# Kernel optimization log

Measured on AMD Instinct MI355X. Metric: run time of the kernel, lower is better.

The kernel has to match this reference:

```python
import jax, jax.numpy as jnp
import numpy as np
import math

NUM_HIDDEN = 512

def setup_inputs() -> dict:
    key = jax.random.key(0)
    k1, k2 = jax.random.split(key)
    a = jax.random.normal(k1, (8, 2048, NUM_HIDDEN), dtype=jnp.float32)
    b = jax.random.normal(k2, (8, 2048, NUM_HIDDEN), dtype=jnp.float32)
    return {"a": a, "b": b}

def reference(a, b):
    # simi_matrix: [B, La, Lb] = a @ b^T / sqrt(H)
    scale = 1.0 / math.sqrt(NUM_HIDDEN)
    simi = jnp.einsum('bld,bmd->blm', a, b) * scale
    norm_weight = jax.nn.softmax(simi, axis=2)
    # up_1: [B, La, H] = attn @ b + residual a
    up_1 = jnp.einsum('blm,bmd->bld', norm_weight, b) + a
    return up_1
```

## Files before the change

kernel.cpp:

```cpp
#include <hip/hip_runtime.h>
#include <hip/hip_bf16.h>

#define D 512
#define NSEQ 2048
#define NB 8
#define QBLK 64
#define KVBLK 64
#define NTHREADS 512
#define NT (NSEQ / KVBLK)
#define ROWE 2112
#define BUFE (16 * ROWE)
#define PROWP 72
#define CROWP 68
#define DEFER_THR 8.0f

typedef __attribute__((ext_vector_type(8))) short bf16x8;
typedef __attribute__((ext_vector_type(4))) float f32x4;
typedef __attribute__((ext_vector_type(4))) unsigned short u16x4;
typedef __attribute__((ext_vector_type(4))) int i32x4;

static __device__ __forceinline__ unsigned short f2b(float f) {
  unsigned u = __builtin_bit_cast(unsigned, f);
  return (unsigned short)((u + 0x7FFFu + ((u >> 16) & 1u)) >> 16);
}

__global__ __launch_bounds__(256) void conv_dual(const float* __restrict__ in,
                                                 unsigned short* __restrict__ b16,
                                                 unsigned short* __restrict__ bT) {
  __shared__ unsigned short tile[64 * CROWP];
  const int bid = blockIdx.x;
  const int batch = bid >> 8;
  const int rem = bid & 255;
  const int kvt = rem >> 3;
  const int dt  = rem & 7;
  const int t = threadIdx.x;
  const int r = t >> 2;
  const int c = (t & 3) * 16;

  const float* src = in + ((size_t)batch * NSEQ + kvt * 64 + r) * D + dt * 64 + c;
  unsigned short* o16 = b16 + ((size_t)batch * NSEQ + kvt * 64 + r) * D + dt * 64 + c;

  float4 v0 = *reinterpret_cast<const float4*>(src);
  float4 v1 = *reinterpret_cast<const float4*>(src + 4);
  float4 v2 = *reinterpret_cast<const float4*>(src + 8);
  float4 v3 = *reinterpret_cast<const float4*>(src + 12);
  bf16x8 h0, h1;
  h0[0] = (short)f2b(v0.x); h0[1] = (short)f2b(v0.y);
  h0[2] = (short)f2b(v0.z); h0[3] = (short)f2b(v0.w);
  h0[4] = (short)f2b(v1.x); h0[5] = (short)f2b(v1.y);
  h0[6] = (short)f2b(v1.z); h0[7] = (short)f2b(v1.w);
  h1[0] = (short)f2b(v2.x); h1[1] = (short)f2b(v2.y);
  h1[2] = (short)f2b(v2.z); h1[3] = (short)f2b(v2.w);
  h1[4] = (short)f2b(v3.x); h1[5] = (short)f2b(v3.y);
  h1[6] = (short)f2b(v3.z); h1[7] = (short)f2b(v3.w);
  *reinterpret_cast<bf16x8*>(o16)     = h0;
  *reinterpret_cast<bf16x8*>(o16 + 8) = h1;
  #pragma unroll
  for (int i = 0; i < 4; ++i) {
    u16x4 w;
    w[0] = (unsigned short)((i < 2 ? h0 : h1)[(i & 1) * 4 + 0]);
    w[1] = (unsigned short)((i < 2 ? h0 : h1)[(i & 1) * 4 + 1]);
    w[2] = (unsigned short)((i < 2 ? h0 : h1)[(i & 1) * 4 + 2]);
    w[3] = (unsigned short)((i < 2 ? h0 : h1)[(i & 1) * 4 + 3]);
    *reinterpret_cast<u16x4*>(&tile[r * CROWP + c + i * 4]) = w;
  }
  __syncthreads();

  const int w  = t >> 6;
  const int dr = t & 63;
  unsigned short* oT = bT + (size_t)batch * D * NSEQ
                          + (size_t)(dt * 64 + dr) * NSEQ + kvt * 64 + w * 16;
  unsigned short g[16];
  #pragma unroll
  for (int i = 0; i < 16; ++i)
    g[i] = tile[(w * 16 + i) * CROWP + dr];
  bf16x8 p0, p1;
  #pragma unroll
  for (int i = 0; i < 8; ++i) { p0[i] = (short)g[i]; p1[i] = (short)g[8 + i]; }
  *reinterpret_cast<bf16x8*>(oT)     = p0;
  *reinterpret_cast<bf16x8*>(oT + 8) = p1;
}

__global__ __launch_bounds__(NTHREADS, 1)
void attn_v18(const float* __restrict__ A, const unsigned short* __restrict__ B16,
              const unsigned short* __restrict__ T16, float* __restrict__ Out) {
  __shared__ __align__(16) unsigned short Bs[BUFE];
  __shared__ __align__(16) unsigned short Bt[D * KVBLK];
  __shared__ __align__(16) unsigned short Ps[QBLK * PROWP];
  __shared__ float mS[QBLK];
  __shared__ float lS[QBLK];
  __shared__ float aS[QBLK];
  __shared__ float pmaxS[128];
  __shared__ float psumS[128];
  __shared__ __align__(16) int flagS[8];

  const int tid  = threadIdx.x;
  const int wid  = tid >> 6;
  const int lane = tid & 63;
  const int l16  = lane & 15;
  const int g4   = lane >> 4;

  const int batch = blockIdx.x & 7;
  const int qt    = blockIdx.x >> 3;
  const int qbase = qt * QBLK;

  const float*          Ab = A   + (size_t)batch * NSEQ * D;
  const unsigned short* Kb = B16 + (size_t)batch * NSEQ * D;
  const unsigned short* Tb = T16 + (size_t)batch * D * NSEQ;
  float*                Ob = Out + (size_t)batch * NSEQ * D;

  const float scale = 0.04419417382415922f;

  const int qi = wid >> 1;
  const int kp = wid & 1;

  const float* Arow = Ab + (size_t)(qbase + qi * 16 + l16) * D;
  bf16x8 qf[16];
  #pragma unroll
  for (int ks = 0; ks < 16; ++ks) {
    int d0 = ks * 32 + g4 * 8;
    float4 v0 = *reinterpret_cast<const float4*>(Arow + d0);
    float4 v1 = *reinterpret_cast<const float4*>(Arow + d0 + 4);
    bf16x8 f;
    f[0] = (short)f2b(v0.x * scale); f[1] = (short)f2b(v0.y * scale);
    f[2] = (short)f2b(v0.z * scale); f[3] = (short)f2b(v0.w * scale);
    f[4] = (short)f2b(v1.x * scale); f[5] = (short)f2b(v1.y * scale);
    f[6] = (short)f2b(v1.z * scale); f[7] = (short)f2b(v1.w * scale);
    qf[ks] = f;
  }
  if (tid < QBLK) { mS[tid] = -1e30f; lS[tid] = 0.f; }

  f32x4 acc[4][4];
  #pragma unroll
  for (int mi = 0; mi < 4; ++mi)
    #pragma unroll
    for (int ni = 0; ni < 4; ++ni)
      acc[mi][ni] = (f32x4){0.f, 0.f, 0.f, 0.f};

  #pragma unroll
  for (int c = 0; c < 8; ++c) {
    int id = wid * 8 + c;
    int g = id >> 2, q = id & 3;
    const unsigned short* src = Kb
        + (size_t)(g * 4 + ((lane >> 1) & 3)) * D
        + q * 128 + (lane >> 3) * 16 + (lane & 1) * 8;
    unsigned short* dst = &Bs[g * ROWE + q * 512];
    __builtin_amdgcn_global_load_lds(
        (const __attribute__((address_space(1))) void*)src,
        (__attribute__((address_space(3))) void*)dst, 16, 0, 0);
  }
  #pragma unroll
  for (int c = 0; c < 8; ++c) {
    int drow = wid * 64 + c * 8 + (lane >> 3);
    int chunk = (lane & 7) ^ ((lane >> 3) & 7);
    const unsigned short* src = Tb + (size_t)drow * NSEQ + chunk * 8;
    unsigned short* dst = (unsigned short*)&Bt[(wid * 64 + c * 8) * KVBLK];
    __builtin_amdgcn_global_load_lds(
        (const __attribute__((address_space(1))) void*)src,
        (__attribute__((address_space(3))) void*)dst, 16, 0, 0);
  }
  asm volatile("s_waitcnt vmcnt(0)" ::: "memory");
  asm volatile("s_waitcnt lgkmcnt(0)" ::: "memory");
  __builtin_amdgcn_s_barrier();

  const int bbase0 = ((kp * 2) * 4 + (l16 >> 2)) * ROWE + (l16 & 3) * 16 + (g4 & 1) * 8;
  const int bbase1 = bbase0 + 4 * ROWE;

  for (int kt = 0; kt < NT; ++kt) {
    f32x4 s0 = {0.f, 0.f, 0.f, 0.f};
    f32x4 s1 = {0.f, 0.f, 0.f, 0.f};
    __builtin_amdgcn_s_setprio(1);
    #pragma unroll
    for (int ks = 0; ks < 16; ++ks) {
      const int ro = (ks * 2 + (g4 >> 1)) * 64;
      const bf16x8 b0 = *reinterpret_cast<const bf16x8*>(&Bs[bbase0 + ro]);
      const bf16x8 b1 = *reinterpret_cast<const bf16x8*>(&Bs[bbase1 + ro]);
      s0 = __builtin_amdgcn_mfma_f32_16x16x32_bf16(b0, qf[ks], s0, 0, 0, 0);
      s1 = __builtin_amdgcn_mfma_f32_16x16x32_bf16(b1, qf[ks], s1, 0, 0, 0);
    }
    __builtin_amdgcn_s_setprio(0);

    {
      float m01 = fmaxf(s0[0], s0[1]), m23 = fmaxf(s0[2], s0[3]);
      float m45 = fmaxf(s1[0], s1[1]), m67 = fmaxf(s1[2], s1[3]);
      float mloc = fmaxf(fmaxf(m01, m23), fmaxf(m45, m67));
      mloc = fmaxf(mloc, __shfl_xor(mloc, 16));
      mloc = fmaxf(mloc, __shfl_xor(mloc, 32));
      if (lane < 16) pmaxS[qi * 32 + kp * 16 + lane] = mloc;
      asm volatile("s_waitcnt lgkmcnt(0)" ::: "memory");
      __builtin_amdgcn_s_barrier();

      if (kt + 1 < NT) {
        const unsigned short* Kt = Kb + (size_t)(kt + 1) * KVBLK * D;
        #pragma unroll
        for (int c = 0; c < 8; ++c) {
          int id = wid * 8 + c;
          int g = id >> 2, q = id & 3;
          const unsigned short* src = Kt
              + (size_t)(g * 4 + ((lane >> 1) & 3)) * D
              + q * 128 + (lane >> 3) * 16 + (lane & 1) * 8;
          unsigned short* dst = &Bs[g * ROWE + q * 512];
          __builtin_amdgcn_global_load_lds(
              (const __attribute__((address_space(1))) void*)src,
              (__attribute__((address_space(3))) void*)dst, 16, 0, 0);
        }
      }

      float mpart = pmaxS[qi * 32 + (kp ^ 1) * 16 + l16];
      float mcomb = fmaxf(mloc, mpart);
      float mold = mS[qi * 16 + l16];
      int defer = (mcomb <= mold + DEFER_THR) ? 1 : 0;
      float mnew = defer ? mold : mcomb;
      float al = defer ? 1.0f : __expf(mold - mnew);

      float rowsum = 0.f;
      u16x4 w0, w1;
      #pragma unroll
      for (int r = 0; r < 4; ++r) {
        float p = __expf(s0[r] - mnew);
        rowsum += p;
        w0[r] = f2b(p);
      }
      #pragma unroll
      for (int r = 0; r < 4; ++r) {
        float p = __expf(s1[r] - mnew);
        rowsum += p;
        w1[r] = f2b(p);
      }
      const int prow = (qi * 16 + l16) * PROWP + 32 * kp + 4 * g4;
      *reinterpret_cast<u16x4*>(&Ps[prow])      = w0;
      *reinterpret_cast<u16x4*>(&Ps[prow + 16]) = w1;

      rowsum += __shfl_xor(rowsum, 16);
      rowsum += __shfl_xor(rowsum, 32);
      if (lane < 16) psumS[qi * 32 + kp * 16 + lane] = rowsum;
      int wave_defer = __all(defer);
      if (kp == 0 && lane < 16) {
        mS[qi * 16 + lane] = mnew;
        aS[qi * 16 + lane] = al;
      }
      if (lane == 0) flagS[wid] = wave_defer;

      asm volatile("s_waitcnt lgkmcnt(0)" ::: "memory");
      if (kt + 1 < NT) {
        asm volatile("s_waitcnt vmcnt(8)" ::: "memory");
      } else {
        asm volatile("s_waitcnt vmcnt(0)" ::: "memory");
      }
      __builtin_amdgcn_s_barrier();

      if (kp == 0 && lane < 16) {
        float pp = psumS[qi * 32 + 16 + lane];
        lS[qi * 16 + lane] = lS[qi * 16 + lane] * al + rowsum + pp;
      }
    }

    {
      i32x4 f0 = *reinterpret_cast<const i32x4*>(&flagS[0]);
      i32x4 f1 = *reinterpret_cast<const i32x4*>(&flagS[4]);
      int allskip = f0[0] & f0[1] & f0[2] & f0[3] & f1[0] & f1[1] & f1[2] & f1[3];
      if (!allskip) {
        #pragma unroll
        for (int mi = 0; mi < 4; ++mi) {
          float a = aS[mi * 16 + l16];
          #pragma unroll
          for (int ni = 0; ni < 4; ++ni)
            #pragma unroll
            for (int r = 0; r < 4; ++r)
              acc[mi][ni][r] *= a;
        }
      }

      const char* Bc = (const char*)&Bt[0];
      __builtin_amdgcn_s_setprio(1);
      #pragma unroll
      for (int ks = 0; ks < 2; ++ks) {
        bf16x8 pf[4];
        #pragma unroll
        for (int mi = 0; mi < 4; ++mi)
          pf[mi] = *reinterpret_cast<const bf16x8*>(
              &Ps[(mi * 16 + l16) * PROWP + ks * 32 + g4 * 8]);
        #pragma unroll
        for (int ni = 0; ni < 4; ++ni) {
          int row = wid * 64 + ni * 16 + l16;
          int swz = (ks * 4 + g4) ^ (l16 & 7);
          const bf16x8 vf = *reinterpret_cast<const bf16x8*>(Bc + row * 128 + swz * 16);
          #pragma unroll
          for (int mi = 0; mi < 4; ++mi)
            acc[mi][ni] = __builtin_amdgcn_mfma_f32_16x16x32_bf16(vf, pf[mi], acc[mi][ni], 0, 0, 0);
        }
      }
      __builtin_amdgcn_s_setprio(0);
    }
    asm volatile("s_waitcnt lgkmcnt(0)" ::: "memory");

    if (kt + 1 < NT) {
      #pragma unroll
      for (int c = 0; c < 8; ++c) {
        int drow = wid * 64 + c * 8 + (lane >> 3);
        int chunk = (lane & 7) ^ ((lane >> 3) & 7);
        const unsigned short* src = Tb + (size_t)drow * NSEQ + (kt + 1) * KVBLK + chunk * 8;
        unsigned short* dst = (unsigned short*)&Bt[(wid * 64 + c * 8) * KVBLK];
        __builtin_amdgcn_global_load_lds(
            (const __attribute__((address_space(1))) void*)src,
            (__attribute__((address_space(3))) void*)dst, 16, 0, 0);
      }
      asm volatile("s_waitcnt vmcnt(8)" ::: "memory");
    }
    __builtin_amdgcn_s_barrier();
  }

  #pragma unroll
  for (int mi = 0; mi < 4; ++mi) {
    float rl = 1.0f / lS[mi * 16 + l16];
    int q = qbase + mi * 16 + l16;
    #pragma unroll
    for (int ni = 0; ni < 4; ++ni) {
      int d = wid * 64 + ni * 16 + g4 * 4;
      const float4 av = *reinterpret_cast<const float4*>(Ab + (size_t)q * D + d);
      float4 o;
      o.x = acc[mi][ni][0] * rl + av.x;
      o.y = acc[mi][ni][1] * rl + av.y;
      o.z = acc[mi][ni][2] * rl + av.z;
      o.w = acc[mi][ni][3] * rl + av.w;
      *reinterpret_cast<float4*>(Ob + (size_t)q * D + d) = o;
    }
  }
}

#define FQBLK 32
#define FSROWP (64 + 4)
#define FPROWP (64 + 8)
__global__ __launch_bounds__(NTHREADS, 2)
void attn_fb(const float* __restrict__ A, const float* __restrict__ B32,
             float* __restrict__ Out) {
  __shared__ __align__(16) unsigned short Bs[BUFE];
  __shared__ float Ss[FQBLK * FSROWP];
  __shared__ unsigned short Ps[FQBLK * FPROWP];
  __shared__ float mS[FQBLK];
  __shared__ float lS[FQBLK];
  __shared__ float aS[FQBLK];

  const int tid  = threadIdx.x;
  const int wid  = tid >> 6;
  const int lane = tid & 63;
  const int l16  = lane & 15;
  const int g4   = lane >> 4;

  const int batch = blockIdx.x & 7;
  const int qt    = blockIdx.x >> 3;
  const int qbase = qt * FQBLK;

  const float* Ab   = A   + (size_t)batch * NSEQ * D;
  const float* Bb32 = B32 + (size_t)batch * NSEQ * D;
  float*       Ob   = Out + (size_t)batch * NSEQ * D;

  const float scale = 0.04419417382415922f;

  const int qi = wid >> 2;
  const int ki = wid & 3;

  const float* Arow = Ab + (size_t)(qbase + qi * 16 + l16) * D;
  bf16x8 qf[16];
  #pragma unroll
  for (int ks = 0; ks < 16; ++ks) {
    int d0 = ks * 32 + g4 * 8;
    float4 v0 = *reinterpret_cast<const float4*>(Arow + d0);
    float4 v1 = *reinterpret_cast<const float4*>(Arow + d0 + 4);
    bf16x8 f;
    f[0] = (short)f2b(v0.x * scale); f[1] = (short)f2b(v0.y * scale);
    f[2] = (short)f2b(v0.z * scale); f[3] = (short)f2b(v0.w * scale);
    f[4] = (short)f2b(v1.x * scale); f[5] = (short)f2b(v1.y * scale);
    f[6] = (short)f2b(v1.z * scale); f[7] = (short)f2b(v1.w * scale);
    qf[ks] = f;
  }
  if (tid < FQBLK) { mS[tid] = -1e30f; lS[tid] = 0.f; }

  f32x4 acc[2][4];
  #pragma unroll
  for (int mi = 0; mi < 2; ++mi)
    #pragma unroll
    for (int ni = 0; ni < 4; ++ni)
      acc[mi][ni] = (f32x4){0.f, 0.f, 0.f, 0.f};

  for (int kt = 0; kt < NT; ++kt) {
    __builtin_amdgcn_s_barrier();
    const float* Bt2 = Bb32 + (size_t)kt * KVBLK * D;
    #pragma unroll
    for (int c = 0; c < 8; ++c) {
      int id = wid * 8 + c;
      int g = id >> 2, q = id & 3;
      int kv = g * 4 + ((lane >> 1) & 3);
      int d  = q * 128 + (lane >> 3) * 16 + (lane & 1) * 8;
      const float* s = Bt2 + (size_t)kv * D + d;
      float4 v0 = *reinterpret_cast<const float4*>(s);
      float4 v1 = *reinterpret_cast<const float4*>(s + 4);
      bf16x8 h;
      h[0] = (short)f2b(v0.x); h[1] = (short)f2b(v0.y);
      h[2] = (short)f2b(v0.z); h[3] = (short)f2b(v0.w);
      h[4] = (short)f2b(v1.x); h[5] = (short)f2b(v1.y);
      h[6] = (short)f2b(v1.z); h[7] = (short)f2b(v1.w);
      *reinterpret_cast<bf16x8*>(&Bs[g * ROWE + q * 512 + lane * 8]) = h;
    }
    asm volatile("s_waitcnt lgkmcnt(0)" ::: "memory");
    __builtin_amdgcn_s_barrier();

    {
      f32x4 s = {0.f, 0.f, 0.f, 0.f};
      const int bbase = (ki * 4 + (l16 >> 2)) * ROWE + (l16 & 3) * 16 + (g4 & 1) * 8;
      #pragma unroll
      for (int ks = 0; ks < 16; ++ks) {
        const bf16x8 bf = *reinterpret_cast<const bf16x8*>(
            &Bs[bbase + (ks * 2 + (g4 >> 1)) * 64]);
        s = __builtin_amdgcn_mfma_f32_16x16x32_bf16(qf[ks], bf, s, 0, 0, 0);
      }
      #pragma unroll
      for (int r = 0; r < 4; ++r)
        Ss[(qi * 16 + g4 * 4 + r) * FSROWP + ki * 16 + l16] = s[r];
    }
    asm volatile("s_waitcnt lgkmcnt(0)" ::: "memory");
    __builtin_amdgcn_s_barrier();

    {
      int row = wid * 4 + g4;
      float sv[4];
      float mloc = -1e30f;
      #pragma unroll
      for (int j = 0; j < 4; ++j) {
        sv[j] = Ss[row * FSROWP + l16 + 16 * j];
        mloc = fmaxf(mloc, sv[j]);
      }
      #pragma unroll
      for (int off = 1; off < 16; off <<= 1)
        mloc = fmaxf(mloc, __shfl_xor(mloc, off));
      float mold = mS[row];
      float mnew = fmaxf(mold, mloc);
      float al = __expf(mold - mnew);
      float psum = 0.f;
      #pragma unroll
      for (int j = 0; j < 4; ++j) {
        float p = __expf(sv[j] - mnew);
        psum += p;
        Ps[row * FPROWP + l16 + 16 * j] = f2b(p);
      }
      #pragma unroll
      for (int off = 1; off < 16; off <<= 1)
        psum += __shfl_xor(psum, off);
      if (l16 == 0) {
        mS[row] = mnew;
        lS[row] = lS[row] * al + psum;
        aS[row] = al;
      }
    }
    asm volatile("s_waitcnt lgkmcnt(0)" ::: "memory");
    __builtin_amdgcn_s_barrier();

    {
      #pragma unroll
      for (int mi = 0; mi < 2; ++mi)
        #pragma unroll
        for (int r = 0; r < 4; ++r) {
          float a = aS[mi * 16 + g4 * 4 + r];
          #pragma unroll
          for (int ni = 0; ni < 4; ++ni)
            acc[mi][ni][r] *= a;
        }

      #pragma unroll
      for (int ks = 0; ks < 2; ++ks) {
        bf16x8 pf[2];
        #pragma unroll
        for (int mi = 0; mi < 2; ++mi)
          pf[mi] = *reinterpret_cast<const bf16x8*>(
              &Ps[(mi * 16 + l16) * FPROWP + ks * 32 + g4 * 8]);
        #pragma unroll
        for (int ni = 0; ni < 4; ++ni) {
          bf16x8 vv;
          #pragma unroll
          for (int j = 0; j < 8; ++j)
            vv[j] = (short)Bs[(ks * 8 + g4 * 2 + (j >> 2)) * ROWE
                              + (wid * 4 + ni) * 64 + (j & 3) * 16 + l16];
          #pragma unroll
          for (int mi = 0; mi < 2; ++mi)
            acc[mi][ni] = __builtin_amdgcn_mfma_f32_16x16x32_bf16(pf[mi], vv, acc[mi][ni], 0, 0, 0);
        }
      }
    }
  }

  #pragma unroll
  for (int mi = 0; mi < 2; ++mi)
    #pragma unroll
    for (int r = 0; r < 4; ++r) {
      float rl = 1.0f / lS[mi * 16 + g4 * 4 + r];
      #pragma unroll
      for (int ni = 0; ni < 4; ++ni) {
        int q = qbase + mi * 16 + g4 * 4 + r;
        int d = wid * 64 + ni * 16 + l16;
        size_t off = (size_t)q * D + d;
        Ob[off] = acc[mi][ni][r] * rl + Ab[off];
      }
    }
}

extern "C" void kernel_launch(void* const* d_in, const int* in_sizes, int n_in,
                              void* d_out, int out_size, void* d_ws, size_t ws_size,
                              hipStream_t stream) {
  const float* a = (const float*)d_in[0];
  const float* b = (const float*)d_in[1];
  float* out = (float*)d_out;
  const size_t one = (size_t)NB * NSEQ * D * sizeof(unsigned short);
  dim3 block(NTHREADS);
  if (ws_size >= 2 * one) {
    unsigned short* b16 = (unsigned short*)d_ws;
    unsigned short* bT  = b16 + (size_t)NB * NSEQ * D;
    conv_dual<<<NB * 256, 256, 0, stream>>>(b, b16, bT);
    dim3 grid(NB * (NSEQ / QBLK));
    attn_v18<<<grid, block, 0, stream>>>(a, b16, bT, out);
  } else {
    dim3 grid(NB * (NSEQ / FQBLK));
    attn_fb<<<grid, block, 0, stream>>>(a, b, out);
  }
}
```

Measured before the change: 131.1 us.

## Remap QK^T wave tiling so each wave shares one K fragment across two query tiles

Each wave now owns one 16-row KV slice and two 16-row query tiles, instead of one query tile and two KV slices. Each LDS read of K feeds two MFMAs, halving K fragment reads from LDS in the score loop. The cost is twice the Q fragments held in registers (32 bf16x8), which raises VGPR pressure. The row max and sum reduction becomes a four-way merge across KV slices through shared memory.

After: 218.0 us. 1.66x slower.

```diff
diff --git a/kernel.cpp b/kernel.cpp
--- a/kernel.cpp
+++ b/kernel.cpp
@@ -82,7 +82,7 @@
 }
 
 __global__ __launch_bounds__(NTHREADS, 1)
-void attn_v18(const float* __restrict__ A, const unsigned short* __restrict__ B16,
+void attn_v19(const float* __restrict__ A, const unsigned short* __restrict__ B16,
               const unsigned short* __restrict__ T16, float* __restrict__ Out) {
   __shared__ __align__(16) unsigned short Bs[BUFE];
   __shared__ __align__(16) unsigned short Bt[D * KVBLK];
@@ -90,8 +90,8 @@
   __shared__ float mS[QBLK];
   __shared__ float lS[QBLK];
   __shared__ float aS[QBLK];
-  __shared__ float pmaxS[128];
-  __shared__ float psumS[128];
+  __shared__ float pmaxS[4 * 64];
+  __shared__ float psumS[4 * 64];
   __shared__ __align__(16) int flagS[8];
 
   const int tid  = threadIdx.x;
@@ -111,22 +111,33 @@
 
   const float scale = 0.04419417382415922f;
 
-  const int qi = wid >> 1;
-  const int kp = wid & 1;
-
-  const float* Arow = Ab + (size_t)(qbase + qi * 16 + l16) * D;
-  bf16x8 qf[16];
-  #pragma unroll
-  for (int ks = 0; ks < 16; ++ks) {
-    int d0 = ks * 32 + g4 * 8;
-    float4 v0 = *reinterpret_cast<const float4*>(Arow + d0);
-    float4 v1 = *reinterpret_cast<const float4*>(Arow + d0 + 4);
-    bf16x8 f;
-    f[0] = (short)f2b(v0.x * scale); f[1] = (short)f2b(v0.y * scale);
-    f[2] = (short)f2b(v0.z * scale); f[3] = (short)f2b(v0.w * scale);
-    f[4] = (short)f2b(v1.x * scale); f[5] = (short)f2b(v1.y * scale);
-    f[6] = (short)f2b(v1.z * scale); f[7] = (short)f2b(v1.w * scale);
-    qf[ks] = f;
+  const int kvt = wid >> 1;
+  const int qp  = wid & 1;
+  const int t0  = qp * 2, t1 = qp * 2 + 1;
+
+  bf16x8 qf0[16], qf1[16];
+  {
+    const float* Ar0 = Ab + (size_t)(qbase + t0 * 16 + l16) * D;
+    const float* Ar1 = Ab + (size_t)(qbase + t1 * 16 + l16) * D;
+    #pragma unroll
+    for (int ks = 0; ks < 16; ++ks) {
+      int d0 = ks * 32 + g4 * 8;
+      float4 a0 = *reinterpret_cast<const float4*>(Ar0 + d0);
+      float4 a1 = *reinterpret_cast<const float4*>(Ar0 + d0 + 4);
+      float4 b0 = *reinterpret_cast<const float4*>(Ar1 + d0);
+      float4 b1 = *reinterpret_cast<const float4*>(Ar1 + d0 + 4);
+      bf16x8 f0, f1;
+      f0[0] = (short)f2b(a0.x * scale); f0[1] = (short)f2b(a0.y * scale);
+      f0[2] = (short)f2b(a0.z * scale); f0[3] = (short)f2b(a0.w * scale);
+      f0[4] = (short)f2b(a1.x * scale); f0[5] = (short)f2b(a1.y * scale);
+      f0[6] = (short)f2b(a1.z * scale); f0[7] = (short)f2b(a1.w * scale);
+      f1[0] = (short)f2b(b0.x * scale); f1[1] = (short)f2b(b0.y * scale);
+      f1[2] = (short)f2b(b0.z * scale); f1[3] = (short)f2b(b0.w * scale);
+      f1[4] = (short)f2b(b1.x * scale); f1[5] = (short)f2b(b1.y * scale);
+      f1[6] = (short)f2b(b1.z * scale); f1[7] = (short)f2b(b1.w * scale);
+      qf0[ks] = f0;
+      qf1[ks] = f1;
+    }
   }
   if (tid < QBLK) { mS[tid] = -1e30f; lS[tid] = 0.f; }
 
@@ -163,8 +174,7 @@
   asm volatile("s_waitcnt lgkmcnt(0)" ::: "memory");
   __builtin_amdgcn_s_barrier();
 
-  const int bbase0 = ((kp * 2) * 4 + (l16 >> 2)) * ROWE + (l16 & 3) * 16 + (g4 & 1) * 8;
-  const int bbase1 = bbase0 + 4 * ROWE;
+  const int bbase = (kvt * 4 + (l16 >> 2)) * ROWE + (l16 & 3) * 16 + (g4 & 1) * 8;
 
   for (int kt = 0; kt < NT; ++kt) {
     f32x4 s0 = {0.f, 0.f, 0.f, 0.f};
@@ -173,86 +183,114 @@
     #pragma unroll
     for (int ks = 0; ks < 16; ++ks) {
       const int ro = (ks * 2 + (g4 >> 1)) * 64;
-      const bf16x8 b0 = *reinterpret_cast<const bf16x8*>(&Bs[bbase0 + ro]);
-      const bf16x8 b1 = *reinterpret_cast<const bf16x8*>(&Bs[bbase1 + ro]);
-      s0 = __builtin_amdgcn_mfma_f32_16x16x32_bf16(b0, qf[ks], s0, 0, 0, 0);
-      s1 = __builtin_amdgcn_mfma_f32_16x16x32_bf16(b1, qf[ks], s1, 0, 0, 0);
+      const bf16x8 b = *reinterpret_cast<const bf16x8*>(&Bs[bbase + ro]);
+      s0 = __builtin_amdgcn_mfma_f32_16x16x32_bf16(b, qf0[ks], s0, 0, 0, 0);
+      s1 = __builtin_amdgcn_mfma_f32_16x16x32_bf16(b, qf1[ks], s1, 0, 0, 0);
     }
     __builtin_amdgcn_s_setprio(0);
 
+    float mloc0, mloc1;
     {
-      float m01 = fmaxf(s0[0], s0[1]), m23 = fmaxf(s0[2], s0[3]);
-      float m45 = fmaxf(s1[0], s1[1]), m67 = fmaxf(s1[2], s1[3]);
-      float mloc = fmaxf(fmaxf(m01, m23), fmaxf(m45, m67));
-      mloc = fmaxf(mloc, __shfl_xor(mloc, 16));
-      mloc = fmaxf(mloc, __shfl_xor(mloc, 32));
-      if (lane < 16) pmaxS[qi * 32 + kp * 16 + lane] = mloc;
-      asm volatile("s_waitcnt lgkmcnt(0)" ::: "memory");
-      __builtin_amdgcn_s_barrier();
-
-      if (kt + 1 < NT) {
-        const unsigned short* Kt = Kb + (size_t)(kt + 1) * KVBLK * D;
-        #pragma unroll
-        for (int c = 0; c < 8; ++c) {
-          int id = wid * 8 + c;
-          int g = id >> 2, q = id & 3;
-          const unsigned short* src = Kt
-              + (size_t)(g * 4 + ((lane >> 1) & 3)) * D
-              + q * 128 + (lane >> 3) * 16 + (lane & 1) * 8;
-          unsigned short* dst = &Bs[g * ROWE + q * 512];
-          __builtin_amdgcn_global_load_lds(
-              (const __attribute__((address_space(1))) void*)src,
-              (__attribute__((address_space(3))) void*)dst, 16, 0, 0);
-        }
-      }
-
-      float mpart = pmaxS[qi * 32 + (kp ^ 1) * 16 + l16];
-      float mcomb = fmaxf(mloc, mpart);
-      float mold = mS[qi * 16 + l16];
-      int defer = (mcomb <= mold + DEFER_THR) ? 1 : 0;
-      float mnew = defer ? mold : mcomb;
-      float al = defer ? 1.0f : __expf(mold - mnew);
-
-      float rowsum = 0.f;
+      float a01 = fmaxf(s0[0], s0[1]), a23 = fmaxf(s0[2], s0[3]);
+      float b01 = fmaxf(s1[0], s1[1]), b23 = fmaxf(s1[2], s1[3]);
+      mloc0 = fmaxf(a01, a23);
+      mloc1 = fmaxf(b01, b23);
+      mloc0 = fmaxf(mloc0, __shfl_xor(mloc0, 16));
+      mloc0 = fmaxf(mloc0, __shfl_xor(mloc0, 32));
+      mloc1 = fmaxf(mloc1, __shfl_xor(mloc1, 16));
+      mloc1 = fmaxf(mloc1, __shfl_xor(mloc1, 32));
+      if (lane < 32) {
+        int t = (lane < 16) ? t0 : t1;
+        float v = (lane < 16) ? mloc0 : mloc1;
+        pmaxS[kvt * 64 + t * 16 + l16] = v;
+      }
+    }
+    asm volatile("s_waitcnt lgkmcnt(0)" ::: "memory");
+    __builtin_amdgcn_s_barrier();
+
+    if (kt + 1 < NT) {
+      const unsigned short* Kt = Kb + (size_t)(kt + 1) * KVBLK * D;
+      #pragma unroll
+      for (int c = 0; c < 8; ++c) {
+        int id = wid * 8 + c;
+        int g = id >> 2, q = id & 3;
+        const unsigned short* src = Kt
+            + (size_t)(g * 4 + ((lane >> 1) & 3)) * D
+            + q * 128 + (lane >> 3) * 16 + (lane & 1) * 8;
+        unsigned short* dst = &Bs[g * ROWE + q * 512];
+        __builtin_amdgcn_global_load_lds(
+            (const __attribute__((address_space(1))) void*)src,
+            (__attribute__((address_space(3))) void*)dst, 16, 0, 0);
+      }
+    }
+
+    float al0, al1, rowsum0, rowsum1;
+    int defer0, defer1;
+    {
+      const int row0 = t0 * 16 + l16, row1 = t1 * 16 + l16;
+      float p0a = pmaxS[0 * 64 + row0], p0b = pmaxS[1 * 64 + row0];
+      float p0c = pmaxS[2 * 64 + row0], p0d = pmaxS[3 * 64 + row0];
+      float p1a = pmaxS[0 * 64 + row1], p1b = pmaxS[1 * 64 + row1];
+      float p1c = pmaxS[2 * 64 + row1], p1d = pmaxS[3 * 64 + row1];
+      float mc0 = fmaxf(fmaxf(p0a, p0b), fmaxf(p0c, p0d));
+      float mc1 = fmaxf(fmaxf(p1a, p1b), fmaxf(p1c, p1d));
+      float mold0 = mS[row0], mold1 = mS[row1];
+      defer0 = (mc0 <= mold0 + DEFER_THR) ? 1 : 0;
+      defer1 = (mc1 <= mold1 + DEFER_THR) ? 1 : 0;
+      float mnew0 = defer0 ? mold0 : mc0;
+      float mnew1 = defer1 ? mold1 : mc1;
+      al0 = defer0 ? 1.0f : __expf(mold0 - mnew0);
+      al1 = defer1 ? 1.0f : __expf(mold1 - mnew1);
+
+      rowsum0 = 0.f; rowsum1 = 0.f;
       u16x4 w0, w1;
       #pragma unroll
       for (int r = 0; r < 4; ++r) {
-        float p = __expf(s0[r] - mnew);
-        rowsum += p;
+        float p = __expf(s0[r] - mnew0);
+        rowsum0 += p;
         w0[r] = f2b(p);
       }
       #pragma unroll
       for (int r = 0; r < 4; ++r) {
-        float p = __expf(s1[r] - mnew);
-        rowsum += p;
+        float p = __expf(s1[r] - mnew1);
+        rowsum1 += p;
         w1[r] = f2b(p);
       }
-      const int prow = (qi * 16 + l16) * PROWP + 32 * kp + 4 * g4;
-      *reinterpret_cast<u16x4*>(&Ps[prow])      = w0;
-      *reinterpret_cast<u16x4*>(&Ps[prow + 16]) = w1;
-
-      rowsum += __shfl_xor(rowsum, 16);
-      rowsum += __shfl_xor(rowsum, 32);
-      if (lane < 16) psumS[qi * 32 + kp * 16 + lane] = rowsum;
-      int wave_defer = __all(defer);
-      if (kp == 0 && lane < 16) {
-        mS[qi * 16 + lane] = mnew;
-        aS[qi * 16 + lane] = al;
+      const int kvoff = kvt * 16 + 4 * g4;
+      *reinterpret_cast<u16x4*>(&Ps[row0 * PROWP + kvoff]) = w0;
+      *reinterpret_cast<u16x4*>(&Ps[row1 * PROWP + kvoff]) = w1;
+
+      rowsum0 += __shfl_xor(rowsum0, 16);
+      rowsum0 += __shfl_xor(rowsum0, 32);
+      rowsum1 += __shfl_xor(rowsum1, 16);
+      rowsum1 += __shfl_xor(rowsum1, 32);
+      if (lane < 32) {
+        int t = (lane < 16) ? t0 : t1;
+        float v = (lane < 16) ? rowsum0 : rowsum1;
+        psumS[kvt * 64 + t * 16 + l16] = v;
+      }
+      int wave_defer = __all(defer0 & defer1);
+      if (kvt == 0 && lane < 32) {
+        int row = ((lane < 16) ? t0 : t1) * 16 + l16;
+        mS[row] = (lane < 16) ? mnew0 : mnew1;
+        aS[row] = (lane < 16) ? al0 : al1;
       }
       if (lane == 0) flagS[wid] = wave_defer;
-
-      asm volatile("s_waitcnt lgkmcnt(0)" ::: "memory");
-      if (kt + 1 < NT) {
-        asm volatile("s_waitcnt vmcnt(8)" ::: "memory");
-      } else {
-        asm volatile("s_waitcnt vmcnt(0)" ::: "memory");
-      }
-      __builtin_amdgcn_s_barrier();
-
-      if (kp == 0 && lane < 16) {
-        float pp = psumS[qi * 32 + 16 + lane];
-        lS[qi * 16 + lane] = lS[qi * 16 + lane] * al + rowsum + pp;
-      }
+    }
+    asm volatile("s_waitcnt lgkmcnt(0)" ::: "memory");
+    if (kt + 1 < NT) {
+      asm volatile("s_waitcnt vmcnt(8)" ::: "memory");
+    } else {
+      asm volatile("s_waitcnt vmcnt(0)" ::: "memory");
+    }
+    __builtin_amdgcn_s_barrier();
+
+    if (kvt == 0 && lane < 32) {
+      int row = ((lane < 16) ? t0 : t1) * 16 + l16;
+      float al = (lane < 16) ? al0 : al1;
+      float sum4 = psumS[0 * 64 + row] + psumS[1 * 64 + row]
+                 + psumS[2 * 64 + row] + psumS[3 * 64 + row];
+      lS[row] = lS[row] * al + sum4;
     }
 
     {
@@ -516,7 +554,7 @@
     unsigned short* bT  = b16 + (size_t)NB * NSEQ * D;
     conv_dual<<<NB * 256, 256, 0, stream>>>(b, b16, bT);
     dim3 grid(NB * (NSEQ / QBLK));
-    attn_v18<<<grid, block, 0, stream>>>(a, b16, bT, out);
+    attn_v19<<<grid, block, 0, stream>>>(a, b16, bT, out);
   } else {
     dim3 grid(NB * (NSEQ / FQBLK));
     attn_fb<<<grid, block, 0, stream>>>(a, b, out);
```
